# Optimization experiments

Hardware: AMD Instinct MI355X
Metric: run time of the kernel (lower is better)

## Reference

```python
import jax, jax.numpy as jnp
import numpy as np

H, W = 256, 256
N = 512
EPS = 1e-4


def setup_inputs() -> dict:
    key = jax.random.key(0)
    k1, k2, k3, k4 = jax.random.split(key, 4)
    means3D = jax.random.normal(k1, (N, 3), dtype=jnp.float32) * 2.0
    # PSD 3D covariances with ~few-pixel projected footprint
    A = jax.random.normal(k2, (N, 3, 3), dtype=jnp.float32) * 0.1
    covs3d = A @ jnp.swapaxes(A, -1, -2)
    colors = jax.random.uniform(k3, (N, 3), dtype=jnp.float32)
    opacities = jax.random.uniform(k4, (N,), dtype=jnp.float32)
    K = jnp.array([[300.0, 0.0, W / 2.0], [0.0, 300.0, H / 2.0], [0.0, 0.0, 1.0]], dtype=jnp.float32)
    R = jnp.eye(3, dtype=jnp.float32)
    t = jnp.array([0.0, 0.0, 10.0], dtype=jnp.float32)
    return dict(means3D=means3D, covs3d=covs3d, colors=colors, opacities=opacities, K=K, R=R, t=t)


def reference(means3D, covs3d, colors, opacities, K, R, t):
    dtype = means3D.dtype
    # --- projection ---
    cam = means3D @ R.T + t[None, :]            # (N,3)
    z = cam[:, 2]
    depths = jnp.clip(z, 1.0)                   # clamp(min=1.0)
    screen = cam @ K.T
    means2D = screen[:, :2] / screen[:, 2:3]    # (N,2)
    fx, fy = K[0, 0], K[1, 1]
    zero = jnp.zeros_like(z)
    # Jacobian rows (row 2 is all zeros, as in the original)
    J = jnp.stack([
        jnp.stack([fx / z, zero, -(fx * cam[:, 0]) / (z * z)], axis=-1),
        jnp.stack([zero, fy / z, -(fy * cam[:, 1]) / (z * z)], axis=-1),
        jnp.stack([zero, zero, zero], axis=-1),
    ], axis=1)                                   # (N,3,3)
    covs_cam = jnp.einsum('ij,njk,lk->nil', R, covs3d, R)       # R Sigma R^T
    covs2D = jnp.einsum('nki,nkl,nlj->nij', J, covs_cam, J)[:, :2, :2]  # J^T Sigma_cam J, top-left 2x2
    valid = (depths > 1.0) & (depths < 50.0)
    # --- depth sort ---
    order = jnp.argsort(depths)
    means2D = means2D[order]
    covs2D = covs2D[order]
    colors_s = colors[order]
    op_s = opacities[order]
    valid = valid[order]
    # --- per-Gaussian pixel evaluation ---
    yy, xx = jnp.meshgrid(jnp.arange(H, dtype=dtype), jnp.arange(W, dtype=dtype), indexing='ij')
    pixels = jnp.stack([xx, yy], axis=-1)                        # (H,W,2)
    dx = pixels[None] - means2D[:, None, None, :]                # (N,H,W,2)
    c = covs2D + EPS * jnp.eye(2, dtype=dtype)
    a, b = c[:, 0, 0], c[:, 0, 1]
    cc, d = c[:, 1, 0], c[:, 1, 1]
    det = a * d - b * cc                                          # (N,)
    inv = jnp.stack([jnp.stack([d, -b], -1), jnp.stack([-cc, a], -1)], axis=1) / det[:, None, None]
    dxi = jnp.einsum('nhwi,nij->nhwj', dx, inv)
    mahal = jnp.sum(dxi * dx, axis=-1)                            # (N,H,W)
    norm = 1.0 / (2.0 * jnp.pi * jnp.sqrt(det))
    gauss = norm[:, None, None] * jnp.exp(-0.5 * mahal)
    gauss = gauss * valid.astype(dtype)[:, None, None]
    # --- front-to-back alpha compositing ---
    alphas = op_s[:, None, None] * gauss                          # (N,H,W)
    T = jnp.cumprod(jnp.concatenate([jnp.ones((1, H, W), dtype=dtype), 1.0 - alphas[:-1]], axis=0), axis=0)
    weights = alphas * T
    rendered = jnp.einsum('nhw,nc->hwc', weights, colors_s)       # (H,W,3)
    return rendered
```

## Files before the change

kernel.cpp:

```cpp
#include <hip/hip_runtime.h>
#include <math.h>

#define IMG_H 256
#define IMG_W 256
#define EPSV 1e-4f
#define SEGS 8
#define PIX_PER_BLK 64
#define SKIP_EPS 1e-7f
#define GPB 64
#define MAXN 2048
#define LOG2E 1.442695041f

#if __has_builtin(__builtin_amdgcn_exp2f)
#define EXP2F(x) __builtin_amdgcn_exp2f(x)
#else
#define EXP2F(x) __expf((x) * 0.6931471805599453f)
#endif

struct __align__(16) GData {
    float4 h0, h1, h2;
};

__global__ __launch_bounds__(512)
void GaussianRenderer_preprocess(const float* __restrict__ means3D,
                                 const float* __restrict__ covs3d,
                                 const float* __restrict__ colors,
                                 const float* __restrict__ opac,
                                 const float* __restrict__ Km,
                                 const float* __restrict__ Rm,
                                 const float* __restrict__ tv,
                                 GData* __restrict__ out, int N)
{
    __shared__ __align__(16) float sdepth[MAXN + 4];
    __shared__ int srank[512];

    const float R00=Rm[0], R01=Rm[1], R02=Rm[2];
    const float R10=Rm[3], R11=Rm[4], R12=Rm[5];
    const float R20=Rm[6], R21=Rm[7], R22=Rm[8];
    const float t2=tv[2];

    const int Npad = (N + 3) & ~3;

    for (int i = threadIdx.x; i < Npad; i += 512) {
        float depth = __builtin_inff();
        if (i < N) {
            const float m0 = means3D[i*3+0], m1 = means3D[i*3+1], m2 = means3D[i*3+2];
            const float z = R20*m0 + R21*m1 + R22*m2 + t2;
            depth = fmaxf(z, 1.0f);
        }
        sdepth[i] = depth;
    }
    __syncthreads();

    {
        const int g   = blockIdx.x * GPB + (threadIdx.x >> 3);
        const int sub = threadIdx.x & 7;
        int rank = 0;
        if (g < N) {
            const float depth = sdepth[g];
            const int total4  = Npad >> 2;
            const int chunk4  = (total4 + 7) >> 3;
            const int b4 = sub * chunk4;
            const int e4 = (b4 + chunk4 < total4) ? (b4 + chunk4) : total4;
            const float4* sd4 = (const float4*)sdepth;
            for (int j4 = b4; j4 < e4; ++j4) {
                const float4 v = sd4[j4];
                const int j = j4 * 4;
                rank += (v.x < depth || (v.x == depth && (j + 0) < g)) ? 1 : 0;
                rank += (v.y < depth || (v.y == depth && (j + 1) < g)) ? 1 : 0;
                rank += (v.z < depth || (v.z == depth && (j + 2) < g)) ? 1 : 0;
                rank += (v.w < depth || (v.w == depth && (j + 3) < g)) ? 1 : 0;
            }
        }
        srank[threadIdx.x] = rank;
    }
    __syncthreads();

    const int t = threadIdx.x;
    const int i = blockIdx.x * GPB + t;
    if (t < GPB && i < N) {
        int rank = 0;
        #pragma unroll
        for (int s = 0; s < 8; ++s) rank += srank[t*8 + s];

        const float K00=Km[0], K01=Km[1], K02=Km[2];
        const float K10=Km[3], K11=Km[4], K12=Km[5];
        const float K20=Km[6], K21=Km[7], K22=Km[8];
        const float fx=Km[0], fy=Km[4];
        const float t0=tv[0], t1=tv[1];

        const float m0 = means3D[i*3+0], m1 = means3D[i*3+1], m2 = means3D[i*3+2];
        const float c0 = R00*m0 + R01*m1 + R02*m2 + t0;
        const float c1 = R10*m0 + R11*m1 + R12*m2 + t1;
        const float c2 = R20*m0 + R21*m1 + R22*m2 + t2;
        const float z = c2;
        const float depth = fmaxf(z, 1.0f);

        const float s0 = K00*c0 + K01*c1 + K02*c2;
        const float s1 = K10*c0 + K11*c1 + K12*c2;
        const float s2 = K20*c0 + K21*c1 + K22*c2;
        const float mx = s0 / s2, my = s1 / s2;

        const float* C = covs3d + i*9;
        const float C00=C[0],C01=C[1],C02=C[2],C10=C[3],C11=C[4],C12=C[5],C20=C[6],C21=C[7],C22=C[8];
        const float M00 = R00*C00 + R01*C10 + R02*C20;
        const float M01 = R00*C01 + R01*C11 + R02*C21;
        const float M02 = R00*C02 + R01*C12 + R02*C22;
        const float M10 = R10*C00 + R11*C10 + R12*C20;
        const float M11 = R10*C01 + R11*C11 + R12*C21;
        const float M12 = R10*C02 + R11*C12 + R12*C22;
        const float S00 = M00*R00 + M01*R01 + M02*R02;
        const float S01 = M00*R10 + M01*R11 + M02*R12;
        const float S10 = M10*R00 + M11*R01 + M12*R02;
        const float S11 = M10*R10 + M11*R11 + M12*R12;

        const float j0 = fx / z, j1 = fy / z;
        const float a  = j0*j0*S00 + EPSV;
        const float b  = j0*S01*j1;
        const float cc = j1*S10*j0;
        const float d  = j1*j1*S11 + EPSV;

        const float det    = a*d - b*cc;
        const float invdet = 1.0f / det;
        const float norm   = 0.15915494309189535f / sqrtf(det);
        const bool valid   = (depth > 1.0f) && (depth < 50.0f);
        const float coeff  = valid ? (opac[i] * norm) : 0.0f;

        float rx2 = -1.0f, ry2 = -1.0f;
        if (coeff > SKIP_EPS) {
            const float L = __logf(coeff * (1.0f / SKIP_EPS));
            rx2 = 2.0f * a * L;
            ry2 = 2.0f * d * L;
        }

        GData gd;
        gd.h0 = make_float4(mx, my, rx2, ry2);
        gd.h1 = make_float4(-0.5f * d * invdet,
                             0.5f * (b + cc) * invdet,
                            -0.5f * a * invdet,
                            coeff);
        gd.h2 = make_float4(colors[i*3+0], colors[i*3+1], colors[i*3+2], 0.f);
        out[rank] = gd;
    }
}

__device__ __forceinline__ float rlane(float v, int n) {
    return __int_as_float(__builtin_amdgcn_readlane(__float_as_int(v), n));
}

__global__ __launch_bounds__(512)
void GaussianRenderer_render(const GData* __restrict__ g,
                             float* __restrict__ out, int N)
{
    const int seg  = __builtin_amdgcn_readfirstlane(threadIdx.x >> 6);
    const int lane = threadIdx.x & 63;
    const int p    = blockIdx.x * PIX_PER_BLK + lane;
    const float px = (float)(p & (IMG_W - 1));
    const float py = (float)(p >> 8);
    const float cx = (float)((blockIdx.x * PIX_PER_BLK) & (IMG_W - 1)) + 31.5f;

    const int segLen = (N + SEGS - 1) / SEGS;
    const int gBeg = seg * segLen;
    const int gEnd = (gBeg + segLen < N) ? (gBeg + segLen) : N;

    float T = 1.0f, ar = 0.0f, ag = 0.0f, ab = 0.0f;

    for (int base = gBeg; base < gEnd; base += 64) {
        const int idx = base + lane;
        float4 h0 = make_float4(0.f, 0.f, -1.f, -1.f);
        float4 h1 = make_float4(0.f, 0.f, 0.f, 0.f);
        float4 h2 = make_float4(0.f, 0.f, 0.f, 0.f);
        if (idx < gEnd) {
            const GData gd = g[idx];
            h0 = gd.h0; h1 = gd.h1; h2 = gd.h2;
        }
        const float dy  = py - h0.y;
        const float qa2 = h1.x * LOG2E;
        const float qb2 = (h1.y * dy) * LOG2E;
        const float lc2 = __logf(h1.w) * LOG2E + ((h1.z * dy) * dy) * LOG2E;

        const float dxm = fmaxf(fabsf(h0.x - cx) - 31.5f, 0.0f);
        const bool hit = (dxm * dxm <= h0.z) && (dy * dy <= h0.w);

        unsigned long long m = __ballot(hit);
        while (m) {
            const int n = __builtin_ctzll(m);
            m &= m - 1;
            const float mx = rlane(h0.x, n);
            const float qa = rlane(qa2,  n);
            const float qb = rlane(qb2,  n);
            const float lc = rlane(lc2,  n);
            const float cr = rlane(h2.x, n);
            const float cg = rlane(h2.y, n);
            const float cb = rlane(h2.z, n);

            const float dx = px - mx;
            const float alpha = EXP2F((qa*dx + qb)*dx + lc);
            const float w = alpha * T;
            ar += w * cr;
            ag += w * cg;
            ab += w * cb;
            T  -= w;
        }
    }

    __shared__ float4 part[SEGS][PIX_PER_BLK];
    part[seg][lane] = make_float4(ar, ag, ab, T);
    __syncthreads();

    if (seg == 0) {
        float Tp = 1.0f, r = 0.0f, gg = 0.0f, b = 0.0f;
        #pragma unroll
        for (int s = 0; s < SEGS; ++s) {
            const float4 v = part[s][lane];
            r  += Tp * v.x;
            gg += Tp * v.y;
            b  += Tp * v.z;
            Tp *= v.w;
        }
        out[p*3 + 0] = r;
        out[p*3 + 1] = gg;
        out[p*3 + 2] = b;
    }
}

extern "C" void kernel_launch(void* const* d_in, const int* in_sizes, int n_in,
                              void* d_out, int out_size, void* d_ws, size_t ws_size,
                              hipStream_t stream)
{
    const float* means3D = (const float*)d_in[0];
    const float* covs3d  = (const float*)d_in[1];
    const float* colors  = (const float*)d_in[2];
    const float* opac    = (const float*)d_in[3];
    const float* Km      = (const float*)d_in[4];
    const float* Rm      = (const float*)d_in[5];
    const float* tv      = (const float*)d_in[6];
    const int N = in_sizes[3];

    GData* gbuf = (GData*)d_ws;

    const int preBlocks = (N + GPB - 1) / GPB;
    GaussianRenderer_preprocess<<<preBlocks, 512, 0, stream>>>(
        means3D, covs3d, colors, opac, Km, Rm, tv, gbuf, N);

    const int total = IMG_H * IMG_W;
    GaussianRenderer_render<<<(total + PIX_PER_BLK - 1) / PIX_PER_BLK, 512, 0, stream>>>(
        gbuf, (float*)d_out, N);
}
```

Baseline: 73.70 us.

## Fuse preprocess and render into one cooperative kernel with grid sync

```diff
diff --git a/kernel.cpp b/kernel.cpp
--- a/kernel.cpp
+++ b/kernel.cpp
@@ -1,5 +1,8 @@
 #include <hip/hip_runtime.h>
+#include <hip/hip_cooperative_groups.h>
 #include <math.h>
+
+namespace cg = cooperative_groups;
 
 #define IMG_H 256
 #define IMG_W 256
@@ -10,6 +13,7 @@
 #define GPB 64
 #define MAXN 2048
 #define LOG2E 1.442695041f
+#define GRID_BLOCKS 256
 
 #if __has_builtin(__builtin_amdgcn_exp2f)
 #define EXP2F(x) __builtin_amdgcn_exp2f(x)
@@ -21,206 +25,212 @@
     float4 h0, h1, h2;
 };
 
-__global__ __launch_bounds__(512)
-void GaussianRenderer_preprocess(const float* __restrict__ means3D,
-                                 const float* __restrict__ covs3d,
-                                 const float* __restrict__ colors,
-                                 const float* __restrict__ opac,
-                                 const float* __restrict__ Km,
-                                 const float* __restrict__ Rm,
-                                 const float* __restrict__ tv,
-                                 GData* __restrict__ out, int N)
+__device__ __forceinline__ float rlane(float v, int n) {
+    return __int_as_float(__builtin_amdgcn_readlane(__float_as_int(v), n));
+}
+
+__global__ __launch_bounds__(512, 2)
+void GaussianRenderer_fused(const float* __restrict__ means3D,
+                            const float* __restrict__ covs3d,
+                            const float* __restrict__ colors,
+                            const float* __restrict__ opac,
+                            const float* __restrict__ Km,
+                            const float* __restrict__ Rm,
+                            const float* __restrict__ tv,
+                            GData* __restrict__ gbuf,
+                            float* __restrict__ out, int N)
 {
     __shared__ __align__(16) float sdepth[MAXN + 4];
     __shared__ int srank[512];
-
-    const float R00=Rm[0], R01=Rm[1], R02=Rm[2];
-    const float R10=Rm[3], R11=Rm[4], R12=Rm[5];
+    __shared__ float4 part[SEGS][PIX_PER_BLK];
+
     const float R20=Rm[6], R21=Rm[7], R22=Rm[8];
     const float t2=tv[2];
 
+    const int preBlocks = (N + GPB - 1) / GPB;
     const int Npad = (N + 3) & ~3;
 
-    for (int i = threadIdx.x; i < Npad; i += 512) {
-        float depth = __builtin_inff();
-        if (i < N) {
+    for (int pb = blockIdx.x; pb < preBlocks; pb += gridDim.x) {
+        const float R00=Rm[0], R01=Rm[1], R02=Rm[2];
+        const float R10=Rm[3], R11=Rm[4], R12=Rm[5];
+
+        for (int i = threadIdx.x; i < Npad; i += 512) {
+            float depth = __builtin_inff();
+            if (i < N) {
+                const float m0 = means3D[i*3+0], m1 = means3D[i*3+1], m2 = means3D[i*3+2];
+                const float z = R20*m0 + R21*m1 + R22*m2 + t2;
+                depth = fmaxf(z, 1.0f);
+            }
+            sdepth[i] = depth;
+        }
+        __syncthreads();
+
+        {
+            const int g   = pb * GPB + (threadIdx.x >> 3);
+            const int sub = threadIdx.x & 7;
+            int rank = 0;
+            if (g < N) {
+                const float depth = sdepth[g];
+                const int total4  = Npad >> 2;
+                const int chunk4  = (total4 + 7) >> 3;
+                const int b4 = sub * chunk4;
+                const int e4 = (b4 + chunk4 < total4) ? (b4 + chunk4) : total4;
+                const float4* sd4 = (const float4*)sdepth;
+                for (int j4 = b4; j4 < e4; ++j4) {
+                    const float4 v = sd4[j4];
+                    const int j = j4 * 4;
+                    rank += (v.x < depth || (v.x == depth && (j + 0) < g)) ? 1 : 0;
+                    rank += (v.y < depth || (v.y == depth && (j + 1) < g)) ? 1 : 0;
+                    rank += (v.z < depth || (v.z == depth && (j + 2) < g)) ? 1 : 0;
+                    rank += (v.w < depth || (v.w == depth && (j + 3) < g)) ? 1 : 0;
+                }
+            }
+            srank[threadIdx.x] = rank;
+        }
+        __syncthreads();
+
+        const int t = threadIdx.x;
+        const int i = pb * GPB + t;
+        if (t < GPB && i < N) {
+            int rank = 0;
+            #pragma unroll
+            for (int s = 0; s < 8; ++s) rank += srank[t*8 + s];
+
+            const float K00=Km[0], K01=Km[1], K02=Km[2];
+            const float K10=Km[3], K11=Km[4], K12=Km[5];
+            const float K20=Km[6], K21=Km[7], K22=Km[8];
+            const float fx=Km[0], fy=Km[4];
+            const float t0=tv[0], t1=tv[1];
+
             const float m0 = means3D[i*3+0], m1 = means3D[i*3+1], m2 = means3D[i*3+2];
-            const float z = R20*m0 + R21*m1 + R22*m2 + t2;
-            depth = fmaxf(z, 1.0f);
-        }
-        sdepth[i] = depth;
+            const float c0 = R00*m0 + R01*m1 + R02*m2 + t0;
+            const float c1 = R10*m0 + R11*m1 + R12*m2 + t1;
+            const float c2 = R20*m0 + R21*m1 + R22*m2 + t2;
+            const float z = c2;
+            const float depth = fmaxf(z, 1.0f);
+
+            const float s0 = K00*c0 + K01*c1 + K02*c2;
+            const float s1 = K10*c0 + K11*c1 + K12*c2;
+            const float s2 = K20*c0 + K21*c1 + K22*c2;
+            const float mx = s0 / s2, my = s1 / s2;
+
+            const float* C = covs3d + i*9;
+            const float C00=C[0],C01=C[1],C02=C[2],C10=C[3],C11=C[4],C12=C[5],C20=C[6],C21=C[7],C22=C[8];
+            const float M00 = R00*C00 + R01*C10 + R02*C20;
+            const float M01 = R00*C01 + R01*C11 + R02*C21;
+            const float M02 = R00*C02 + R01*C12 + R02*C22;
+            const float M10 = R10*C00 + R11*C10 + R12*C20;
+            const float M11 = R10*C01 + R11*C11 + R12*C21;
+            const float M12 = R10*C02 + R11*C12 + R12*C22;
+            const float S00 = M00*R00 + M01*R01 + M02*R02;
+            const float S01 = M00*R10 + M01*R11 + M02*R12;
+            const float S10 = M10*R00 + M11*R01 + M12*R02;
+            const float S11 = M10*R10 + M11*R11 + M12*R12;
+
+            const float j0 = fx / z, j1 = fy / z;
+            const float a  = j0*j0*S00 + EPSV;
+            const float b  = j0*S01*j1;
+            const float cc = j1*S10*j0;
+            const float d  = j1*j1*S11 + EPSV;
+
+            const float det    = a*d - b*cc;
+            const float invdet = 1.0f / det;
+            const float norm   = 0.15915494309189535f / sqrtf(det);
+            const bool valid   = (depth > 1.0f) && (depth < 50.0f);
+            const float coeff  = valid ? (opac[i] * norm) : 0.0f;
+
+            float rx2 = -1.0f, ry2 = -1.0f;
+            if (coeff > SKIP_EPS) {
+                const float L = __logf(coeff * (1.0f / SKIP_EPS));
+                rx2 = 2.0f * a * L;
+                ry2 = 2.0f * d * L;
+            }
+
+            GData gd;
+            gd.h0 = make_float4(mx, my, rx2, ry2);
+            gd.h1 = make_float4(-0.5f * d * invdet,
+                                 0.5f * (b + cc) * invdet,
+                                -0.5f * a * invdet,
+                                coeff);
+            gd.h2 = make_float4(colors[i*3+0], colors[i*3+1], colors[i*3+2], 0.f);
+            gbuf[rank] = gd;
+        }
     }
-    __syncthreads();
-
-    {
-        const int g   = blockIdx.x * GPB + (threadIdx.x >> 3);
-        const int sub = threadIdx.x & 7;
-        int rank = 0;
-        if (g < N) {
-            const float depth = sdepth[g];
-            const int total4  = Npad >> 2;
-            const int chunk4  = (total4 + 7) >> 3;
-            const int b4 = sub * chunk4;
-            const int e4 = (b4 + chunk4 < total4) ? (b4 + chunk4) : total4;
-            const float4* sd4 = (const float4*)sdepth;
-            for (int j4 = b4; j4 < e4; ++j4) {
-                const float4 v = sd4[j4];
-                const int j = j4 * 4;
-                rank += (v.x < depth || (v.x == depth && (j + 0) < g)) ? 1 : 0;
-                rank += (v.y < depth || (v.y == depth && (j + 1) < g)) ? 1 : 0;
-                rank += (v.z < depth || (v.z == depth && (j + 2) < g)) ? 1 : 0;
-                rank += (v.w < depth || (v.w == depth && (j + 3) < g)) ? 1 : 0;
-            }
-        }
-        srank[threadIdx.x] = rank;
-    }
-    __syncthreads();
-
-    const int t = threadIdx.x;
-    const int i = blockIdx.x * GPB + t;
-    if (t < GPB && i < N) {
-        int rank = 0;
-        #pragma unroll
-        for (int s = 0; s < 8; ++s) rank += srank[t*8 + s];
-
-        const float K00=Km[0], K01=Km[1], K02=Km[2];
-        const float K10=Km[3], K11=Km[4], K12=Km[5];
-        const float K20=Km[6], K21=Km[7], K22=Km[8];
-        const float fx=Km[0], fy=Km[4];
-        const float t0=tv[0], t1=tv[1];
-
-        const float m0 = means3D[i*3+0], m1 = means3D[i*3+1], m2 = means3D[i*3+2];
-        const float c0 = R00*m0 + R01*m1 + R02*m2 + t0;
-        const float c1 = R10*m0 + R11*m1 + R12*m2 + t1;
-        const float c2 = R20*m0 + R21*m1 + R22*m2 + t2;
-        const float z = c2;
-        const float depth = fmaxf(z, 1.0f);
-
-        const float s0 = K00*c0 + K01*c1 + K02*c2;
-        const float s1 = K10*c0 + K11*c1 + K12*c2;
-        const float s2 = K20*c0 + K21*c1 + K22*c2;
-        const float mx = s0 / s2, my = s1 / s2;
-
-        const float* C = covs3d + i*9;
-        const float C00=C[0],C01=C[1],C02=C[2],C10=C[3],C11=C[4],C12=C[5],C20=C[6],C21=C[7],C22=C[8];
-        const float M00 = R00*C00 + R01*C10 + R02*C20;
-        const float M01 = R00*C01 + R01*C11 + R02*C21;
-        const float M02 = R00*C02 + R01*C12 + R02*C22;
-        const float M10 = R10*C00 + R11*C10 + R12*C20;
-        const float M11 = R10*C01 + R11*C11 + R12*C21;
-        const float M12 = R10*C02 + R11*C12 + R12*C22;
-        const float S00 = M00*R00 + M01*R01 + M02*R02;
-        const float S01 = M00*R10 + M01*R11 + M02*R12;
-        const float S10 = M10*R00 + M11*R01 + M12*R02;
-        const float S11 = M10*R10 + M11*R11 + M12*R12;
-
-        const float j0 = fx / z, j1 = fy / z;
-        const float a  = j0*j0*S00 + EPSV;
-        const float b  = j0*S01*j1;
-        const float cc = j1*S10*j0;
-        const float d  = j1*j1*S11 + EPSV;
-
-        const float det    = a*d - b*cc;
-        const float invdet = 1.0f / det;
-        const float norm   = 0.15915494309189535f / sqrtf(det);
-        const bool valid   = (depth > 1.0f) && (depth < 50.0f);
-        const float coeff  = valid ? (opac[i] * norm) : 0.0f;
-
-        float rx2 = -1.0f, ry2 = -1.0f;
-        if (coeff > SKIP_EPS) {
-            const float L = __logf(coeff * (1.0f / SKIP_EPS));
-            rx2 = 2.0f * a * L;
-            ry2 = 2.0f * d * L;
-        }
-
-        GData gd;
-        gd.h0 = make_float4(mx, my, rx2, ry2);
-        gd.h1 = make_float4(-0.5f * d * invdet,
-                             0.5f * (b + cc) * invdet,
-                            -0.5f * a * invdet,
-                            coeff);
-        gd.h2 = make_float4(colors[i*3+0], colors[i*3+1], colors[i*3+2], 0.f);
-        out[rank] = gd;
-    }
-}
-
-__device__ __forceinline__ float rlane(float v, int n) {
-    return __int_as_float(__builtin_amdgcn_readlane(__float_as_int(v), n));
-}
-
-__global__ __launch_bounds__(512)
-void GaussianRenderer_render(const GData* __restrict__ g,
-                             float* __restrict__ out, int N)
-{
+
+    cg::this_grid().sync();
+
     const int seg  = __builtin_amdgcn_readfirstlane(threadIdx.x >> 6);
     const int lane = threadIdx.x & 63;
-    const int p    = blockIdx.x * PIX_PER_BLK + lane;
-    const float px = (float)(p & (IMG_W - 1));
-    const float py = (float)(p >> 8);
-    const float cx = (float)((blockIdx.x * PIX_PER_BLK) & (IMG_W - 1)) + 31.5f;
-
     const int segLen = (N + SEGS - 1) / SEGS;
     const int gBeg = seg * segLen;
     const int gEnd = (gBeg + segLen < N) ? (gBeg + segLen) : N;
-
-    float T = 1.0f, ar = 0.0f, ag = 0.0f, ab = 0.0f;
-
-    for (int base = gBeg; base < gEnd; base += 64) {
-        const int idx = base + lane;
-        float4 h0 = make_float4(0.f, 0.f, -1.f, -1.f);
-        float4 h1 = make_float4(0.f, 0.f, 0.f, 0.f);
-        float4 h2 = make_float4(0.f, 0.f, 0.f, 0.f);
-        if (idx < gEnd) {
-            const GData gd = g[idx];
-            h0 = gd.h0; h1 = gd.h1; h2 = gd.h2;
-        }
-        const float dy  = py - h0.y;
-        const float qa2 = h1.x * LOG2E;
-        const float qb2 = (h1.y * dy) * LOG2E;
-        const float lc2 = __logf(h1.w) * LOG2E + ((h1.z * dy) * dy) * LOG2E;
-
-        const float dxm = fmaxf(fabsf(h0.x - cx) - 31.5f, 0.0f);
-        const bool hit = (dxm * dxm <= h0.z) && (dy * dy <= h0.w);
-
-        unsigned long long m = __ballot(hit);
-        while (m) {
-            const int n = __builtin_ctzll(m);
-            m &= m - 1;
-            const float mx = rlane(h0.x, n);
-            const float qa = rlane(qa2,  n);
-            const float qb = rlane(qb2,  n);
-            const float lc = rlane(lc2,  n);
-            const float cr = rlane(h2.x, n);
-            const float cg = rlane(h2.y, n);
-            const float cb = rlane(h2.z, n);
-
-            const float dx = px - mx;
-            const float alpha = EXP2F((qa*dx + qb)*dx + lc);
-            const float w = alpha * T;
-            ar += w * cr;
-            ag += w * cg;
-            ab += w * cb;
-            T  -= w;
-        }
-    }
-
-    __shared__ float4 part[SEGS][PIX_PER_BLK];
-    part[seg][lane] = make_float4(ar, ag, ab, T);
-    __syncthreads();
-
-    if (seg == 0) {
-        float Tp = 1.0f, r = 0.0f, gg = 0.0f, b = 0.0f;
-        #pragma unroll
-        for (int s = 0; s < SEGS; ++s) {
-            const float4 v = part[s][lane];
-            r  += Tp * v.x;
-            gg += Tp * v.y;
-            b  += Tp * v.z;
-            Tp *= v.w;
-        }
-        out[p*3 + 0] = r;
-        out[p*3 + 1] = gg;
-        out[p*3 + 2] = b;
+    const int nStrips = (IMG_H * IMG_W) / PIX_PER_BLK;
+
+    for (int strip = blockIdx.x; strip < nStrips; strip += gridDim.x) {
+        const int p    = strip * PIX_PER_BLK + lane;
+        const float px = (float)(p & (IMG_W - 1));
+        const float py = (float)(p >> 8);
+        const float cx = (float)((strip * PIX_PER_BLK) & (IMG_W - 1)) + 31.5f;
+
+        float T = 1.0f, ar = 0.0f, ag = 0.0f, ab = 0.0f;
+
+        for (int base = gBeg; base < gEnd; base += 64) {
+            const int idx = base + lane;
+            float4 h0 = make_float4(0.f, 0.f, -1.f, -1.f);
+            float4 h1 = make_float4(0.f, 0.f, 0.f, 0.f);
+            float4 h2 = make_float4(0.f, 0.f, 0.f, 0.f);
+            if (idx < gEnd) {
+                const GData gd = gbuf[idx];
+                h0 = gd.h0; h1 = gd.h1; h2 = gd.h2;
+            }
+            const float dy  = py - h0.y;
+            const float qa2 = h1.x * LOG2E;
+            const float qb2 = (h1.y * dy) * LOG2E;
+            const float lc2 = __logf(h1.w) * LOG2E + ((h1.z * dy) * dy) * LOG2E;
+
+            const float dxm = fmaxf(fabsf(h0.x - cx) - 31.5f, 0.0f);
+            const bool hit = (dxm * dxm <= h0.z) && (dy * dy <= h0.w);
+
+            unsigned long long m = __ballot(hit);
+            while (m) {
+                const int n = __builtin_ctzll(m);
+                m &= m - 1;
+                const float mx = rlane(h0.x, n);
+                const float qa = rlane(qa2,  n);
+                const float qb = rlane(qb2,  n);
+                const float lc = rlane(lc2,  n);
+                const float cr = rlane(h2.x, n);
+                const float cg_ = rlane(h2.y, n);
+                const float cb = rlane(h2.z, n);
+
+                const float dx = px - mx;
+                const float alpha = EXP2F((qa*dx + qb)*dx + lc);
+                const float w = alpha * T;
+                ar += w * cr;
+                ag += w * cg_;
+                ab += w * cb;
+                T  -= w;
+            }
+        }
+
+        __syncthreads();
+        part[seg][lane] = make_float4(ar, ag, ab, T);
+        __syncthreads();
+
+        if (seg == 0) {
+            float Tp = 1.0f, r = 0.0f, gg = 0.0f, b = 0.0f;
+            #pragma unroll
+            for (int s = 0; s < SEGS; ++s) {
+                const float4 v = part[s][lane];
+                r  += Tp * v.x;
+                gg += Tp * v.y;
+                b  += Tp * v.z;
+                Tp *= v.w;
+            }
+            out[p*3 + 0] = r;
+            out[p*3 + 1] = gg;
+            out[p*3 + 2] = b;
+        }
     }
 }
 
@@ -235,15 +245,15 @@
     const float* Km      = (const float*)d_in[4];
     const float* Rm      = (const float*)d_in[5];
     const float* tv      = (const float*)d_in[6];
-    const int N = in_sizes[3];
+    int N = in_sizes[3];
 
     GData* gbuf = (GData*)d_ws;
-
-    const int preBlocks = (N + GPB - 1) / GPB;
-    GaussianRenderer_preprocess<<<preBlocks, 512, 0, stream>>>(
-        means3D, covs3d, colors, opac, Km, Rm, tv, gbuf, N);
-
-    const int total = IMG_H * IMG_W;
-    GaussianRenderer_render<<<(total + PIX_PER_BLK - 1) / PIX_PER_BLK, 512, 0, stream>>>(
-        gbuf, (float*)d_out, N);
+    float* outp = (float*)d_out;
+
+    void* args[] = { (void*)&means3D, (void*)&covs3d, (void*)&colors,
+                     (void*)&opac, (void*)&Km, (void*)&Rm, (void*)&tv,
+                     (void*)&gbuf, (void*)&outp, (void*)&N };
+
+    hipLaunchCooperativeKernel((const void*)GaussianRenderer_fused,
+                               dim3(GRID_BLOCKS), dim3(512), args, 0, stream);
 }
```

Measured after the change: 111.8 us. 51.7% more time.
